# Optimization experiments

Hardware: AMD Instinct MI355X
Metric: run time of the kernel (lower is better)

## Reference

```python
import jax, jax.numpy as jnp
import numpy as np

D = 1024      # in_features
H = 8         # heads per branch (head_num // 2)
DH = (D // 2) // H  # 64
OUT = 1024

def _split_heads(x, B, S):
    # [B, S, D/2] -> [B, H, S, DH]
    return x.reshape(B, S, H, DH).transpose(0, 2, 1, 3)

def _attn(q, k, v):
    # q,k,v: [B, H, S, DH]
    scores = jnp.einsum('bhqd,bhkd->bhqk', q, k) / jnp.sqrt(jnp.float32(DH))
    a = jax.nn.softmax(scores, axis=-1)
    return jnp.einsum('bhqk,bhkd->bhqd', a, v)

def setup_inputs() -> dict:
    key = jax.random.key(0)
    ks = jax.random.split(key, 16)
    B, S = 2, 2048
    d2 = D // 2
    sc = lambda fan_in: 1.0 / np.sqrt(fan_in)
    inp = {
        'f1': jax.random.normal(ks[0], (B, S, D), jnp.float32),
        'f2': jax.random.normal(ks[1], (B, S, D), jnp.float32),
    }
    names = ['qs', 'ks', 'vs', 'qc', 'kc', 'vc']
    for i, n in enumerate(names):
        inp['W' + n] = jax.random.uniform(ks[2 + i], (d2, D), jnp.float32, -sc(D), sc(D))
        inp['b' + n] = jax.random.uniform(ks[8 + i], (d2,), jnp.float32, -sc(D), sc(D))
    inp['Wo'] = jax.random.uniform(ks[14], (OUT, 2 * D), jnp.float32, -sc(2 * D), sc(2 * D))
    inp['bo'] = jax.random.uniform(ks[15], (OUT,), jnp.float32, -sc(2 * D), sc(2 * D))
    return inp

def reference(f1, f2, Wqs, bqs, Wks, bks, Wvs, bvs, Wqc, bqc, Wkc, bkc, Wvc, bvc, Wo, bo):
    B, S, _ = f1.shape
    lin = lambda x, W, b: jax.nn.relu(x @ W.T + b)
    qs = lin(f1, Wqs, bqs); ks_ = lin(f1, Wks, bks); vs = lin(f1, Wvs, bvs)
    qc = lin(f1, Wqc, bqc); kc = lin(f2, Wkc, bkc); vc = lin(f2, Wvc, bvc)
    ys = _attn(_split_heads(qs, B, S), _split_heads(ks_, B, S), _split_heads(vs, B, S))
    yc = _attn(_split_heads(qc, B, S), _split_heads(kc, B, S), _split_heads(vc, B, S))
    merge = lambda y: y.transpose(0, 2, 1, 3).reshape(B, S, D // 2)
    # reshape_to_batches followed by reshape_from_batches on vs/vc is identity
    y = jnp.concatenate([merge(ys), merge(yc), vs, vc], axis=-1)  # [B, S, 2D]
    return jax.nn.relu(y @ Wo.T + bo)
```

## Files before the change

### kernel.cpp

```cpp
#include <hip/hip_runtime.h>
#include <hip/hip_bf16.h>

using bf16 = __hip_bfloat16;
typedef __attribute__((ext_vector_type(8))) short bf16x8;
typedef __attribute__((ext_vector_type(4))) float f32x4;

#define MTOT 4096

__device__ __forceinline__ f32x4 fzero() {
    f32x4 z = {0.f, 0.f, 0.f, 0.f};
    return z;
}

__device__ __forceinline__ f32x4 mfma16(bf16x8 a, bf16x8 b, f32x4 c) {
    return __builtin_amdgcn_mfma_f32_16x16x32_bf16(a, b, c, 0, 0, 0);
}

typedef const __attribute__((address_space(1))) unsigned int* gas_ptr;
typedef __attribute__((address_space(3))) unsigned int* las_ptr;
__device__ __forceinline__ void async_copy16(const bf16* g, bf16* l) {
    __builtin_amdgcn_global_load_lds((gas_ptr)(const void*)g, (las_ptr)(void*)l, 16, 0, 0);
}

__device__ __forceinline__ bf16x8 load8(const bf16* p) {
    return *(const bf16x8*)p;
}
__device__ __forceinline__ bf16x8 load8(const float* p) {
    float4 a = *(const float4*)p;
    float4 b = *(const float4*)(p + 4);
    bf16 t[8];
    t[0] = __float2bfloat16(a.x); t[1] = __float2bfloat16(a.y);
    t[2] = __float2bfloat16(a.z); t[3] = __float2bfloat16(a.w);
    t[4] = __float2bfloat16(b.x); t[5] = __float2bfloat16(b.y);
    t[6] = __float2bfloat16(b.z); t[7] = __float2bfloat16(b.w);
    return *(const bf16x8*)t;
}

__device__ __forceinline__ void store_out(bf16* C, size_t idx, float v) {
    C[idx] = __float2bfloat16(v);
}
__device__ __forceinline__ void store_out(float* C, size_t idx, float v) {
    C[idx] = v;
}

__global__ void MultiHeadSelfCrossAttention_7834020348638_kernel(float* out, int n) {
    int i = blockIdx.x * blockDim.x + threadIdx.x;
    if (i < n) out[i] = 0.25f;
}

struct CvtArgs {
    const float* src[9];
    bf16* dst[9];
    int n8[9];
};
__global__ void cvt_kernel(CvtArgs a) {
    int seg = blockIdx.y;
    int t = blockIdx.x * blockDim.x + threadIdx.x;
    if (t < a.n8[seg])
        *(bf16x8*)(a.dst[seg] + (size_t)t * 8) = load8(a.src[seg] + (size_t)t * 8);
}

template <int BN, typename TC>
__device__ __forceinline__ void gemm_fast(
    const bf16* __restrict__ A, int lda,
    const bf16* __restrict__ Bt, int ldb,
    const float* __restrict__ bias,
    TC* __restrict__ C, int ldc,
    int K, int m0, int n0)
{
    constexpr int NI  = BN / 32;
    constexpr int ACH = 128 * 64 / 8 / 256;
    constexpr int BCH = BN * 64 / 8 / 256;

    __shared__ bf16 As[128 * 64];
    __shared__ bf16 Bs[BN * 64];

    const int tid  = threadIdx.x;
    const int lane = tid & 63;
    const int l15  = lane & 15, quad = lane >> 4;
    const int wave = tid >> 6;
    const int wr   = wave >> 1, wc = wave & 1;

    f32x4 acc[4][NI];
#pragma unroll
    for (int mi = 0; mi < 4; mi++)
#pragma unroll
        for (int ni = 0; ni < NI; ni++)
            acc[mi][ni] = fzero();

    for (int k0 = 0; k0 < K; k0 += 64) {
        __syncthreads();
#pragma unroll
        for (int i = 0; i < ACH; i++) {
            int idx = i * 256 + tid;
            int r   = idx >> 3;
            int cg  = (idx & 7) * 8;
            async_copy16(A + (size_t)(m0 + r) * lda + k0 + cg, &As[idx * 8]);
        }
#pragma unroll
        for (int i = 0; i < BCH; i++) {
            int idx = i * 256 + tid;
            int r   = idx >> 3;
            int cg  = (idx & 7) * 8;
            async_copy16(Bt + (size_t)(n0 + r) * ldb + k0 + cg, &Bs[idx * 8]);
        }
        __syncthreads();

#pragma unroll
        for (int ks = 0; ks < 2; ks++) {
            bf16x8 af[4], bfr[NI];
#pragma unroll
            for (int mi = 0; mi < 4; mi++)
                af[mi] = *(const bf16x8*)&As[(wr * 64 + mi * 16 + l15) * 64 + ks * 32 + quad * 8];
#pragma unroll
            for (int ni = 0; ni < NI; ni++)
                bfr[ni] = *(const bf16x8*)&Bs[(wc * (BN / 2) + ni * 16 + l15) * 64 + ks * 32 + quad * 8];
#pragma unroll
            for (int mi = 0; mi < 4; mi++)
#pragma unroll
                for (int ni = 0; ni < NI; ni++)
                    acc[mi][ni] = mfma16(af[mi], bfr[ni], acc[mi][ni]);
        }
    }

#pragma unroll
    for (int ni = 0; ni < NI; ni++) {
        int col = n0 + wc * (BN / 2) + ni * 16 + l15;
        float bb = bias[col];
#pragma unroll
        for (int mi = 0; mi < 4; mi++) {
#pragma unroll
            for (int r = 0; r < 4; r++) {
                int row = m0 + wr * 64 + mi * 16 + quad * 4 + r;
                store_out(C, (size_t)row * ldc + col, fmaxf(acc[mi][ni][r] + bb, 0.f));
            }
        }
    }
}

template <int BN, typename TA, typename TB, typename TC>
__device__ __forceinline__ void gemm_reg(
    const TA* __restrict__ A, int lda,
    const TB* __restrict__ Bt, int ldb,
    const float* __restrict__ bias,
    TC* __restrict__ C, int ldc,
    int K, int m0, int n0)
{
    constexpr int NI  = BN / 32;
    constexpr int BCH = BN * 4 / 256;

    __shared__ bf16 As[128 * 32];
    __shared__ bf16 Bs[BN * 32];

    const int tid  = threadIdx.x;
    const int lane = tid & 63;
    const int l15  = lane & 15, quad = lane >> 4;
    const int wave = tid >> 6;
    const int wr   = wave >> 1, wc = wave & 1;

    f32x4 acc[4][NI];
#pragma unroll
    for (int mi = 0; mi < 4; mi++)
#pragma unroll
        for (int ni = 0; ni < NI; ni++)
            acc[mi][ni] = fzero();

    for (int k0 = 0; k0 < K; k0 += 32) {
        bf16x8 ra[2], rb[BCH];
#pragma unroll
        for (int i = 0; i < 2; i++) {
            int idx = i * 256 + tid;
            ra[i] = load8(A + (size_t)(m0 + (idx >> 2)) * lda + k0 + (idx & 3) * 8);
        }
#pragma unroll
        for (int i = 0; i < BCH; i++) {
            int idx = i * 256 + tid;
            rb[i] = load8(Bt + (size_t)(n0 + (idx >> 2)) * ldb + k0 + (idx & 3) * 8);
        }
        __syncthreads();
#pragma unroll
        for (int i = 0; i < 2; i++)
            *(bf16x8*)&As[(i * 256 + tid) * 8] = ra[i];
#pragma unroll
        for (int i = 0; i < BCH; i++)
            *(bf16x8*)&Bs[(i * 256 + tid) * 8] = rb[i];
        __syncthreads();

        bf16x8 af[4], bfr[NI];
#pragma unroll
        for (int mi = 0; mi < 4; mi++)
            af[mi] = *(const bf16x8*)&As[(wr * 64 + mi * 16 + l15) * 32 + quad * 8];
#pragma unroll
        for (int ni = 0; ni < NI; ni++)
            bfr[ni] = *(const bf16x8*)&Bs[(wc * (BN / 2) + ni * 16 + l15) * 32 + quad * 8];
#pragma unroll
        for (int mi = 0; mi < 4; mi++)
#pragma unroll
            for (int ni = 0; ni < NI; ni++)
                acc[mi][ni] = mfma16(af[mi], bfr[ni], acc[mi][ni]);
    }

#pragma unroll
    for (int ni = 0; ni < NI; ni++) {
        int col = n0 + wc * (BN / 2) + ni * 16 + l15;
        float bb = bias[col];
#pragma unroll
        for (int mi = 0; mi < 4; mi++) {
#pragma unroll
            for (int r = 0; r < 4; r++) {
                int row = m0 + wr * 64 + mi * 16 + quad * 4 + r;
                store_out(C, (size_t)row * ldc + col, fmaxf(acc[mi][ni][r] + bb, 0.f));
            }
        }
    }
}

__global__ void proj_fast(
    const bf16* __restrict__ F1, const bf16* __restrict__ F2,
    const bf16* __restrict__ Wb,
    const float* __restrict__ bqs, const float* __restrict__ bks,
    const float* __restrict__ bvs, const float* __restrict__ bqc,
    const float* __restrict__ bkc, const float* __restrict__ bvc,
    bf16* __restrict__ Y, bf16* Qs, bf16* Ks, bf16* Qc, bf16* Kc)
{
    const int g = blockIdx.z;
    const bf16* X; const float* bi; bf16* C; int ldc;
    switch (g) {
        case 0:  X = F1; bi = bqs; C = Qs;       ldc = 512;  break;
        case 1:  X = F1; bi = bks; C = Ks;       ldc = 512;  break;
        case 2:  X = F1; bi = bvs; C = Y + 1024; ldc = 2048; break;
        case 3:  X = F1; bi = bqc; C = Qc;       ldc = 512;  break;
        case 4:  X = F2; bi = bkc; C = Kc;       ldc = 512;  break;
        default: X = F2; bi = bvc; C = Y + 1536; ldc = 2048; break;
    }
    gemm_fast<128, bf16>(X, 1024, Wb + (size_t)g * 512 * 1024, 1024, bi, C, ldc,
                         1024, blockIdx.y * 128, blockIdx.x * 128);
}

__global__ void out_fast(const bf16* __restrict__ Y, const bf16* __restrict__ WoB,
                         const float* __restrict__ bo, float* __restrict__ out)
{
    gemm_fast<64, float>(Y, 2048, WoB, 2048, bo, out, 1024, 2048,
                         blockIdx.y * 128, blockIdx.x * 64);
}

__global__ void proj_reg(
    const float* __restrict__ f1, const float* __restrict__ f2,
    const float* __restrict__ Wqs, const float* __restrict__ bqs,
    const float* __restrict__ Wks, const float* __restrict__ bks,
    const float* __restrict__ Wvs, const float* __restrict__ bvs,
    const float* __restrict__ Wqc, const float* __restrict__ bqc,
    const float* __restrict__ Wkc, const float* __restrict__ bkc,
    const float* __restrict__ Wvc, const float* __restrict__ bvc,
    bf16* __restrict__ Y, bf16* Qs, bf16* Ks, bf16* Qc, bf16* Kc)
{
    const int g = blockIdx.z;
    const float *X, *W, *bi; bf16* C; int ldc;
    switch (g) {
        case 0:  X = f1; W = Wqs; bi = bqs; C = Qs;       ldc = 512;  break;
        case 1:  X = f1; W = Wks; bi = bks; C = Ks;       ldc = 512;  break;
        case 2:  X = f1; W = Wvs; bi = bvs; C = Y + 1024; ldc = 2048; break;
        case 3:  X = f1; W = Wqc; bi = bqc; C = Qc;       ldc = 512;  break;
        case 4:  X = f2; W = Wkc; bi = bkc; C = Kc;       ldc = 512;  break;
        default: X = f2; W = Wvc; bi = bvc; C = Y + 1536; ldc = 2048; break;
    }
    gemm_reg<128>(X, 1024, W, 1024, bi, C, ldc, 1024, blockIdx.y * 128, blockIdx.x * 128);
}

__global__ void out_reg(const bf16* __restrict__ Y, const float* __restrict__ Wo,
                        const float* __restrict__ bo, float* __restrict__ out)
{
    gemm_reg<64>(Y, 2048, Wo, 2048, bo, out, 1024, 2048, blockIdx.y * 128, blockIdx.x * 64);
}

__global__ void vt_kernel(const bf16* __restrict__ Y, bf16* __restrict__ VT) {
    const int tid = threadIdx.x;
    const int st = blockIdx.x, bh = blockIdx.y, br = blockIdx.z;
    const int b = bh >> 3, h = bh & 7;
    const bf16* src = Y + (size_t)b * 2048 * 2048 + 1024 + br * 512 + h * 64;
    bf16* dst = VT + ((size_t)((br * 2 + b) * 8 + h)) * 64 * 2048;
    const int s0 = st * 64;
#pragma unroll
    for (int i = 0; i < 2; i++) {
        int idx = i * 256 + tid;
        int d = idx >> 3, cs = (idx & 7) * 8;
        bf16 tmp[8];
#pragma unroll
        for (int j = 0; j < 8; j++)
            tmp[j] = src[(size_t)(s0 + cs + j) * 2048 + d];
        *(bf16x8*)&dst[(size_t)d * 2048 + s0 + cs] = *(const bf16x8*)tmp;
    }
}

__global__ __launch_bounds__(256, 2) void attn2_kernel(
    const bf16* __restrict__ Qsb, const bf16* __restrict__ Ksb,
    const bf16* __restrict__ Qcb, const bf16* __restrict__ Kcb,
    const bf16* __restrict__ VT, bf16* __restrict__ Y)
{
    __shared__ bf16 Kbuf[2][64 * 64];
    __shared__ bf16 Vbuf[2][64 * 64];
    __shared__ bf16 QP[128 * 72];

    const int tid  = threadIdx.x;
    const int lane = tid & 63;
    const int l15  = lane & 15, quad = lane >> 4;
    const int wave = tid >> 6;
    const int qt = blockIdx.x, bh = blockIdx.y, br = blockIdx.z;
    const int b = bh >> 3, h = bh & 7;

    const bf16* Qb = (br ? Qcb : Qsb) + (size_t)b * 2048 * 512 + h * 64;
    const bf16* Kb = (br ? Kcb : Ksb) + (size_t)b * 2048 * 512 + h * 64;
    const bf16* Vt = VT + ((size_t)((br * 2 + b) * 8 + h)) * 64 * 2048;
    bf16*       Ob = Y + (size_t)b * 2048 * 2048 + br * 512 + h * 64;
    const int q0 = qt * 128;

#pragma unroll
    for (int i = 0; i < 4; i++) {
        int idx = i * 256 + tid;
        int r = idx >> 3, c0 = (idx & 7) * 8;
        *(bf16x8*)&QP[r * 72 + c0] = *(const bf16x8*)&Qb[(size_t)(q0 + r) * 512 + c0];
    }

#pragma unroll
    for (int i = 0; i < 2; i++) {
        int idx = i * 256 + tid;
        int r = idx >> 3, sl = (idx & 7) ^ (r & 7);
        async_copy16(Kb + (size_t)r * 512 + sl * 8, &Kbuf[0][idx * 8]);
    }
#pragma unroll
    for (int i = 0; i < 2; i++) {
        int idx = i * 256 + tid;
        int r = idx >> 3, sl = (idx & 7) ^ (r & 7);
        async_copy16(Vt + (size_t)r * 2048 + sl * 8, &Vbuf[0][idx * 8]);
    }
    __syncthreads();

    bf16x8 qf[2][2];
#pragma unroll
    for (int m = 0; m < 2; m++)
#pragma unroll
        for (int ks = 0; ks < 2; ks++)
            qf[m][ks] = *(const bf16x8*)&QP[(wave * 32 + m * 16 + l15) * 72 + ks * 32 + quad * 8];

    const short one_bits = l15 == 0 ? (short)0x3F80 : (short)0;
    bf16x8 onesf;
#pragma unroll
    for (int j = 0; j < 8; j++) onesf[j] = one_bits;

    f32x4 o[2][4], ol[2];
#pragma unroll
    for (int m = 0; m < 2; m++) {
        ol[m] = fzero();
#pragma unroll
        for (int ni = 0; ni < 4; ni++) o[m][ni] = fzero();
    }

    for (int jt = 0; jt < 32; jt++) {
        const int cur = jt & 1;

        if (jt < 31) {
            const size_t s0n = (size_t)(jt + 1) * 64;
#pragma unroll
            for (int i = 0; i < 2; i++) {
                int idx = i * 256 + tid;
                int r = idx >> 3, sl = (idx & 7) ^ (r & 7);
                async_copy16(Kb + (s0n + r) * 512 + sl * 8, &Kbuf[cur ^ 1][idx * 8]);
            }
#pragma unroll
            for (int i = 0; i < 2; i++) {
                int idx = i * 256 + tid;
                int r = idx >> 3, sl = (idx & 7) ^ (r & 7);
                async_copy16(Vt + (size_t)r * 2048 + s0n + sl * 8, &Vbuf[cur ^ 1][idx * 8]);
            }
        }

        f32x4 s[2][4];
#pragma unroll
        for (int m = 0; m < 2; m++)
#pragma unroll
            for (int ni = 0; ni < 4; ni++) s[m][ni] = fzero();
#pragma unroll
        for (int ni = 0; ni < 4; ni++)
#pragma unroll
            for (int ks = 0; ks < 2; ks++) {
                bf16x8 kf = *(const bf16x8*)&Kbuf[cur][(ni * 16 + l15) * 64
                               + (((ks * 4 + quad) ^ (l15 & 7)) * 8)];
#pragma unroll
                for (int m = 0; m < 2; m++)
                    s[m][ni] = mfma16(qf[m][ks], kf, s[m][ni]);
            }

#pragma unroll
        for (int m = 0; m < 2; m++)
#pragma unroll
            for (int ni = 0; ni < 4; ni++)
#pragma unroll
                for (int r = 0; r < 4; r++) {
                    float p = __expf(s[m][ni][r] * 0.125f - 4.0f);
                    QP[(wave * 32 + m * 16 + quad * 4 + r) * 72 + ni * 16 + l15] =
                        __float2bfloat16(p);
                }

#pragma unroll
        for (int ks = 0; ks < 2; ks++) {
            bf16x8 pf[2];
#pragma unroll
            for (int m = 0; m < 2; m++)
                pf[m] = *(const bf16x8*)&QP[(wave * 32 + m * 16 + l15) * 72 + ks * 32 + quad * 8];
#pragma unroll
            for (int ni = 0; ni < 4; ni++) {
                bf16x8 vf = *(const bf16x8*)&Vbuf[cur][(ni * 16 + l15) * 64
                               + (((ks * 4 + quad) ^ (l15 & 7)) * 8)];
#pragma unroll
                for (int m = 0; m < 2; m++)
                    o[m][ni] = mfma16(pf[m], vf, o[m][ni]);
            }
#pragma unroll
            for (int m = 0; m < 2; m++)
                ol[m] = mfma16(pf[m], onesf, ol[m]);
        }

        __syncthreads();
    }

#pragma unroll
    for (int m = 0; m < 2; m++)
#pragma unroll
        for (int r = 0; r < 4; r++) {
            float lsum = __shfl(ol[m][r], quad << 4);
            float inv = 1.f / lsum;
            int row = q0 + wave * 32 + m * 16 + quad * 4 + r;
#pragma unroll
            for (int ni = 0; ni < 4; ni++)
                Ob[(size_t)row * 2048 + ni * 16 + l15] = __float2bfloat16(o[m][ni][r] * inv);
        }
}

__global__ __launch_bounds__(256, 4) void attn_kernel(
    const bf16* __restrict__ Qsb, const bf16* __restrict__ Ksb,
    const bf16* __restrict__ Qcb, const bf16* __restrict__ Kcb,
    bf16* __restrict__ Y)
{
    __shared__ bf16 QP[64 * 72];
    __shared__ bf16 Ksh[64 * 72];
    __shared__ bf16 Vsh[64 * 72];

    const int tid  = threadIdx.x;
    const int lane = tid & 63;
    const int l15  = lane & 15, quad = lane >> 4;
    const int wave = tid >> 6;
    const int qt = blockIdx.x, bh = blockIdx.y, br = blockIdx.z;
    const int b = bh >> 3, h = bh & 7;

    const bf16* Qb = (br ? Qcb : Qsb) + (size_t)b * 2048 * 512 + h * 64;
    const bf16* Kb = (br ? Kcb : Ksb) + (size_t)b * 2048 * 512 + h * 64;
    const bf16* Vb = Y + (size_t)b * 2048 * 2048 + 1024 + br * 512 + h * 64;
    bf16*       Ob = Y + (size_t)b * 2048 * 2048 +        br * 512 + h * 64;
    const int q0 = qt * 64;

#pragma unroll
    for (int i = 0; i < 2; i++) {
        int idx = i * 256 + tid;
        int r = idx >> 3, c0 = (idx & 7) * 8;
        *(bf16x8*)&QP[r * 72 + c0] = *(const bf16x8*)&Qb[(size_t)(q0 + r) * 512 + c0];
    }
    __syncthreads();

    bf16x8 qf[2];
#pragma unroll
    for (int ks = 0; ks < 2; ks++)
        qf[ks] = *(const bf16x8*)&QP[(wave * 16 + l15) * 72 + ks * 32 + quad * 8];

    const short one_bits = l15 == 0 ? (short)0x3F80 : (short)0;
    bf16x8 onesf;
#pragma unroll
    for (int j = 0; j < 8; j++) onesf[j] = one_bits;

    f32x4 o[4], o_l;
    o_l = fzero();
#pragma unroll
    for (int ni = 0; ni < 4; ni++) o[ni] = fzero();

    const int kr0 = tid >> 3, kc0 = (tid & 7) * 8;
    const int kr1 = (256 + tid) >> 3;

    bf16x8 kr[2], vr[2];
    kr[0] = *(const bf16x8*)&Kb[(size_t)kr0 * 512 + kc0];
    kr[1] = *(const bf16x8*)&Kb[(size_t)kr1 * 512 + kc0];
    vr[0] = *(const bf16x8*)&Vb[(size_t)lane * 2048 + (0 * 4 + wave) * 8];
    vr[1] = *(const bf16x8*)&Vb[(size_t)lane * 2048 + (1 * 4 + wave) * 8];

    for (int jt = 0; jt < 32; jt++) {
        __syncthreads();
        *(bf16x8*)&Ksh[kr0 * 72 + kc0] = kr[0];
        *(bf16x8*)&Ksh[kr1 * 72 + kc0] = kr[1];
#pragma unroll
        for (int i = 0; i < 2; i++) {
            int cg = i * 4 + wave;
            const bf16* e = (const bf16*)&vr[i];
#pragma unroll
            for (int j = 0; j < 8; j++)
                Vsh[(cg * 8 + j) * 72 + lane] = e[j];
        }
        __syncthreads();

        {
            const int s0n = (jt < 31) ? (jt + 1) * 64 : 31 * 64;
            kr[0] = *(const bf16x8*)&Kb[(size_t)(s0n + kr0) * 512 + kc0];
            kr[1] = *(const bf16x8*)&Kb[(size_t)(s0n + kr1) * 512 + kc0];
            vr[0] = *(const bf16x8*)&Vb[(size_t)(s0n + lane) * 2048 + (0 * 4 + wave) * 8];
            vr[1] = *(const bf16x8*)&Vb[(size_t)(s0n + lane) * 2048 + (1 * 4 + wave) * 8];
        }

        f32x4 s[4];
#pragma unroll
        for (int ni = 0; ni < 4; ni++) s[ni] = fzero();
#pragma unroll
        for (int ni = 0; ni < 4; ni++)
#pragma unroll
            for (int ks = 0; ks < 2; ks++) {
                bf16x8 kf = *(const bf16x8*)&Ksh[(ni * 16 + l15) * 72 + ks * 32 + quad * 8];
                s[ni] = mfma16(qf[ks], kf, s[ni]);
            }

#pragma unroll
        for (int ni = 0; ni < 4; ni++)
#pragma unroll
            for (int r = 0; r < 4; r++) {
                float p = __expf(s[ni][r] * 0.125f - 4.0f);
                QP[(wave * 16 + quad * 4 + r) * 72 + ni * 16 + l15] = __float2bfloat16(p);
            }

#pragma unroll
        for (int ks = 0; ks < 2; ks++) {
            bf16x8 pf = *(const bf16x8*)&QP[(wave * 16 + l15) * 72 + ks * 32 + quad * 8];
#pragma unroll
            for (int ni = 0; ni < 4; ni++) {
                bf16x8 vf = *(const bf16x8*)&Vsh[(ni * 16 + l15) * 72 + ks * 32 + quad * 8];
                o[ni] = mfma16(pf, vf, o[ni]);
            }
            o_l = mfma16(pf, onesf, o_l);
        }
    }

#pragma unroll
    for (int r = 0; r < 4; r++) {
        float lsum = __shfl(o_l[r], quad << 4);
        float inv = 1.f / lsum;
        int row = q0 + wave * 16 + quad * 4 + r;
#pragma unroll
        for (int ni = 0; ni < 4; ni++)
            Ob[(size_t)row * 2048 + ni * 16 + l15] = __float2bfloat16(o[ni][r] * inv);
    }
}

extern "C" void kernel_launch(void* const* d_in, const int* in_sizes, int n_in,
                              void* d_out, int out_size, void* d_ws, size_t ws_size,
                              hipStream_t stream) {
    const size_t out_bytes = (size_t)out_size * sizeof(float);
    const size_t ws_base = ((size_t)MTOT * 2048 + 4 * (size_t)MTOT * 512) * 2;
    const size_t ws_fast = ws_base + ((size_t)2 * MTOT * 1024 + 6 * 512 * 1024 + 1024 * 2048) * 2;
    const size_t vt_elems = (size_t)2 * 2 * 8 * 64 * 2048;
    const size_t ws_fast2 = ws_fast + vt_elems * 2;

    if (n_in != 16) { hipMemsetAsync(d_out, 0x43, out_bytes, stream); return; }
    if (ws_size < ws_base) { hipMemsetAsync(d_out, 0x41, out_bytes, stream); return; }

    const float* f1  = (const float*)d_in[0];
    const float* f2  = (const float*)d_in[1];
    const float* Wqs = (const float*)d_in[2];  const float* bqs = (const float*)d_in[3];
    const float* Wks = (const float*)d_in[4];  const float* bks = (const float*)d_in[5];
    const float* Wvs = (const float*)d_in[6];  const float* bvs = (const float*)d_in[7];
    const float* Wqc = (const float*)d_in[8];  const float* bqc = (const float*)d_in[9];
    const float* Wkc = (const float*)d_in[10]; const float* bkc = (const float*)d_in[11];
    const float* Wvc = (const float*)d_in[12]; const float* bvc = (const float*)d_in[13];
    const float* Wo  = (const float*)d_in[14]; const float* bo  = (const float*)d_in[15];

    bf16* Y  = (bf16*)d_ws;
    bf16* Qs = Y  + (size_t)MTOT * 2048;
    bf16* Ks = Qs + (size_t)MTOT * 512;
    bf16* Qc = Ks + (size_t)MTOT * 512;
    bf16* Kc = Qc + (size_t)MTOT * 512;
    float* out = (float*)d_out;

    if (ws_size >= ws_fast) {
        bf16* F1  = Kc + (size_t)MTOT * 512;
        bf16* F2  = F1 + (size_t)MTOT * 1024;
        bf16* Wb  = F2 + (size_t)MTOT * 1024;
        bf16* WoB = Wb + (size_t)6 * 512 * 1024;
        bf16* VT  = WoB + (size_t)1024 * 2048;

        CvtArgs ca;
        ca.src[0] = f1;  ca.dst[0] = F1;  ca.n8[0] = MTOT * 1024 / 8;
        ca.src[1] = f2;  ca.dst[1] = F2;  ca.n8[1] = MTOT * 1024 / 8;
        const float* ws_[6] = {Wqs, Wks, Wvs, Wqc, Wkc, Wvc};
        for (int i = 0; i < 6; i++) {
            ca.src[2 + i] = ws_[i];
            ca.dst[2 + i] = Wb + (size_t)i * 512 * 1024;
            ca.n8[2 + i]  = 512 * 1024 / 8;
        }
        ca.src[8] = Wo; ca.dst[8] = WoB; ca.n8[8] = 1024 * 2048 / 8;

        cvt_kernel<<<dim3((MTOT * 1024 / 8 + 255) / 256, 9), 256, 0, stream>>>(ca);
        proj_fast<<<dim3(4, 32, 6), 256, 0, stream>>>(
            F1, F2, Wb, bqs, bks, bvs, bqc, bkc, bvc, Y, Qs, Ks, Qc, Kc);
        if (ws_size >= ws_fast2) {
            vt_kernel<<<dim3(32, 16, 2), 256, 0, stream>>>(Y, VT);
            attn2_kernel<<<dim3(16, 16, 2), 256, 0, stream>>>(Qs, Ks, Qc, Kc, VT, Y);
        } else {
            attn_kernel<<<dim3(32, 16, 2), 256, 0, stream>>>(Qs, Ks, Qc, Kc, Y);
        }
        out_fast<<<dim3(16, 32), 256, 0, stream>>>(Y, WoB, bo, out);
    } else {
        proj_reg<<<dim3(4, 32, 6), 256, 0, stream>>>(
            f1, f2, Wqs, bqs, Wks, bks, Wvs, bvs, Wqc, bqc, Wkc, bkc, Wvc, bvc,
            Y, Qs, Ks, Qc, Kc);
        attn_kernel<<<dim3(32, 16, 2), 256, 0, stream>>>(Qs, Ks, Qc, Kc, Y);
        out_reg<<<dim3(16, 32), 256, 0, stream>>>(Y, Wo, bo, out);
    }
}
```

Baseline: 252.1 us.

## Switch attention to 32x32 MFMA with register-resident P and XCD-aware block mapping

The attention kernel now uses 32x32x16 bf16 MFMA and computes S transposed (K·Q), so exponentiated probabilities can be packed into bf16 and exchanged between lane halves with permlane32 swaps. This removes the LDS round trip for P. Block indices are remapped so blocks sharing a head and branch land on the same XCD, which should improve L2 reuse of K/V. The output is staged through shared memory to allow coalesced 16-byte stores, at the cost of an extra sync and relying on inline asm specific to gfx950.

```diff
diff --git a/kernel.cpp b/kernel.cpp
--- a/kernel.cpp
+++ b/kernel.cpp
@@ -4,6 +4,8 @@
 using bf16 = __hip_bfloat16;
 typedef __attribute__((ext_vector_type(8))) short bf16x8;
 typedef __attribute__((ext_vector_type(4))) float f32x4;
+typedef __attribute__((ext_vector_type(16))) float f32x16;
+typedef __attribute__((ext_vector_type(4))) unsigned int u32x4;
 
 #define MTOT 4096
 
@@ -11,9 +13,16 @@
     f32x4 z = {0.f, 0.f, 0.f, 0.f};
     return z;
 }
+__device__ __forceinline__ f32x16 fzero16() {
+    f32x16 z = {0.f,0.f,0.f,0.f,0.f,0.f,0.f,0.f,0.f,0.f,0.f,0.f,0.f,0.f,0.f,0.f};
+    return z;
+}
 
 __device__ __forceinline__ f32x4 mfma16(bf16x8 a, bf16x8 b, f32x4 c) {
     return __builtin_amdgcn_mfma_f32_16x16x32_bf16(a, b, c, 0, 0, 0);
+}
+__device__ __forceinline__ f32x16 mfma32(bf16x8 a, bf16x8 b, f32x16 c) {
+    return __builtin_amdgcn_mfma_f32_32x32x16_bf16(a, b, c, 0, 0, 0);
 }
 
 typedef const __attribute__((address_space(1))) unsigned int* gas_ptr;
@@ -303,9 +312,15 @@
 
     const int tid  = threadIdx.x;
     const int lane = tid & 63;
-    const int l15  = lane & 15, quad = lane >> 4;
+    const int l31  = lane & 31;
+    const int hi   = lane >> 5;
     const int wave = tid >> 6;
-    const int qt = blockIdx.x, bh = blockIdx.y, br = blockIdx.z;
+
+    const int lid   = blockIdx.x + 16 * blockIdx.y + 256 * blockIdx.z;
+    const int xcd   = lid & 7, slot = lid >> 3;
+    const int combo = xcd + 8 * (slot >> 4);
+    const int qt    = slot & 15;
+    const int bh    = combo & 15, br = combo >> 4;
     const int b = bh >> 3, h = bh & 7;
 
     const bf16* Qb = (br ? Qcb : Qsb) + (size_t)b * 2048 * 512 + h * 64;
@@ -335,25 +350,18 @@
     }
     __syncthreads();
 
-    bf16x8 qf[2][2];
-#pragma unroll
-    for (int m = 0; m < 2; m++)
-#pragma unroll
-        for (int ks = 0; ks < 2; ks++)
-            qf[m][ks] = *(const bf16x8*)&QP[(wave * 32 + m * 16 + l15) * 72 + ks * 32 + quad * 8];
-
-    const short one_bits = l15 == 0 ? (short)0x3F80 : (short)0;
-    bf16x8 onesf;
-#pragma unroll
-    for (int j = 0; j < 8; j++) onesf[j] = one_bits;
-
-    f32x4 o[2][4], ol[2];
-#pragma unroll
-    for (int m = 0; m < 2; m++) {
-        ol[m] = fzero();
-#pragma unroll
-        for (int ni = 0; ni < 4; ni++) o[m][ni] = fzero();
-    }
+    bf16x8 qf[4];
+#pragma unroll
+    for (int kq = 0; kq < 4; kq++)
+        qf[kq] = *(const bf16x8*)&QP[(wave * 32 + l31) * 72 + kq * 16 + hi * 8];
+
+    const short one_bits = (l31 == 0) ? (short)0x3F80 : (short)0;
+    bf16x8 onesA;
+#pragma unroll
+    for (int j = 0; j < 8; j++) onesA[j] = one_bits;
+
+    f32x16 o[2], ol;
+    o[0] = fzero16(); o[1] = fzero16(); ol = fzero16();
 
     for (int jt = 0; jt < 32; jt++) {
         const int cur = jt & 1;
@@ -374,66 +382,68 @@
             }
         }
 
-        f32x4 s[2][4];
-#pragma unroll
-        for (int m = 0; m < 2; m++)
-#pragma unroll
-            for (int ni = 0; ni < 4; ni++) s[m][ni] = fzero();
-#pragma unroll
-        for (int ni = 0; ni < 4; ni++)
-#pragma unroll
-            for (int ks = 0; ks < 2; ks++) {
-                bf16x8 kf = *(const bf16x8*)&Kbuf[cur][(ni * 16 + l15) * 64
-                               + (((ks * 4 + quad) ^ (l15 & 7)) * 8)];
-#pragma unroll
-                for (int m = 0; m < 2; m++)
-                    s[m][ni] = mfma16(qf[m][ks], kf, s[m][ni]);
-            }
-
-#pragma unroll
-        for (int m = 0; m < 2; m++)
-#pragma unroll
-            for (int ni = 0; ni < 4; ni++)
-#pragma unroll
-                for (int r = 0; r < 4; r++) {
-                    float p = __expf(s[m][ni][r] * 0.125f - 4.0f);
-                    QP[(wave * 32 + m * 16 + quad * 4 + r) * 72 + ni * 16 + l15] =
-                        __float2bfloat16(p);
-                }
-
-#pragma unroll
-        for (int ks = 0; ks < 2; ks++) {
-            bf16x8 pf[2];
-#pragma unroll
-            for (int m = 0; m < 2; m++)
-                pf[m] = *(const bf16x8*)&QP[(wave * 32 + m * 16 + l15) * 72 + ks * 32 + quad * 8];
-#pragma unroll
-            for (int ni = 0; ni < 4; ni++) {
-                bf16x8 vf = *(const bf16x8*)&Vbuf[cur][(ni * 16 + l15) * 64
-                               + (((ks * 4 + quad) ^ (l15 & 7)) * 8)];
-#pragma unroll
-                for (int m = 0; m < 2; m++)
-                    o[m][ni] = mfma16(pf[m], vf, o[m][ni]);
-            }
-#pragma unroll
-            for (int m = 0; m < 2; m++)
-                ol[m] = mfma16(pf[m], onesf, ol[m]);
+        f32x16 st[2];
+        st[0] = fzero16(); st[1] = fzero16();
+#pragma unroll
+        for (int t = 0; t < 2; t++)
+#pragma unroll
+            for (int kq = 0; kq < 4; kq++) {
+                bf16x8 kf = *(const bf16x8*)&Kbuf[cur][(t * 32 + l31) * 64
+                               + (((kq * 2 + hi) ^ (l31 & 7)) * 8)];
+                st[t] = mfma32(kf, qf[kq], st[t]);
+            }
+
+        unsigned int pk[2][4][2];
+#pragma unroll
+        for (int t = 0; t < 2; t++)
+#pragma unroll
+            for (int g = 0; g < 4; g++) {
+                float e0 = __expf(st[t][4 * g + 0] * 0.125f - 4.0f);
+                float e1 = __expf(st[t][4 * g + 1] * 0.125f - 4.0f);
+                float e2 = __expf(st[t][4 * g + 2] * 0.125f - 4.0f);
+                float e3 = __expf(st[t][4 * g + 3] * 0.125f - 4.0f);
+                asm("v_cvt_pk_bf16_f32 %0, %1, %2"
+                    : "=v"(pk[t][g][0]) : "v"(e0), "v"(e1));
+                asm("v_cvt_pk_bf16_f32 %0, %1, %2"
+                    : "=v"(pk[t][g][1]) : "v"(e2), "v"(e3));
+            }
+
+#pragma unroll
+        for (int kb = 0; kb < 4; kb++) {
+            const int t = kb >> 1, gb = (kb & 1) * 2;
+            unsigned int u0 = pk[t][gb][0],     u1 = pk[t][gb][1];
+            unsigned int v0 = pk[t][gb + 1][0], v1 = pk[t][gb + 1][1];
+            asm("v_permlane32_swap_b32 %0, %1" : "+v"(u0), "+v"(v0));
+            asm("v_permlane32_swap_b32 %0, %1" : "+v"(u1), "+v"(v1));
+            u32x4 pw; pw.x = u0; pw.y = u1; pw.z = v0; pw.w = v1;
+            bf16x8 pfrag = __builtin_bit_cast(bf16x8, pw);
+#pragma unroll
+            for (int dt = 0; dt < 2; dt++) {
+                bf16x8 vf = *(const bf16x8*)&Vbuf[cur][(dt * 32 + l31) * 64
+                               + (((kb * 2 + hi) ^ (l31 & 7)) * 8)];
+                o[dt] = mfma32(vf, pfrag, o[dt]);
+            }
+            ol = mfma32(onesA, pfrag, ol);
         }
 
         __syncthreads();
     }
 
-#pragma unroll
-    for (int m = 0; m < 2; m++)
-#pragma unroll
-        for (int r = 0; r < 4; r++) {
-            float lsum = __shfl(ol[m][r], quad << 4);
-            float inv = 1.f / lsum;
-            int row = q0 + wave * 32 + m * 16 + quad * 4 + r;
-#pragma unroll
-            for (int ni = 0; ni < 4; ni++)
-                Ob[(size_t)row * 2048 + ni * 16 + l15] = __float2bfloat16(o[m][ni][r] * inv);
-        }
+    const float linv = 1.0f / __shfl(ol[0], l31);
+#pragma unroll
+    for (int dt = 0; dt < 2; dt++)
+#pragma unroll
+        for (int r = 0; r < 16; r++) {
+            int d = dt * 32 + (r & 3) + 8 * (r >> 2) + 4 * hi;
+            QP[(wave * 32 + l31) * 72 + d] = __float2bfloat16(o[dt][r] * linv);
+        }
+    __syncthreads();
+#pragma unroll
+    for (int i = 0; i < 4; i++) {
+        int idx = i * 256 + tid;
+        int r = idx >> 3, c0 = (idx & 7) * 8;
+        *(bf16x8*)&Ob[(size_t)(q0 + r) * 2048 + c0] = *(const bf16x8*)&QP[r * 72 + c0];
+    }
 }
 
 __global__ __launch_bounds__(256, 4) void attn_kernel(
```

New measurement: 244.6 us. 1.03x faster.
